# Kernel optimization log

Hardware: AMD Instinct MI355X
Metric: run time of the kernel (lower is better)

## Reference

```python
import jax, jax.numpy as jnp
import numpy as np

INPUT_SIZE = 1024
OUTPUT_SIZE = 1024
B, S = 4, 2048


def setup_inputs() -> dict:
    key = jax.random.key(0)
    k1, k2, k3, k4, k5, k6 = jax.random.split(key, 6)
    scale = 1.0 / np.sqrt(INPUT_SIZE)
    return {
        "inputs_for_keys": jax.random.normal(k1, (B, S, INPUT_SIZE), jnp.float32),
        "inputs_for_values": jax.random.normal(k2, (B, S, INPUT_SIZE), jnp.float32),
        "inputs_for_queries": jax.random.normal(k3, (B, S, INPUT_SIZE), jnp.float32),
        "W_k": jax.random.normal(k4, (INPUT_SIZE, OUTPUT_SIZE), jnp.float32) * scale,
        "W_v": jax.random.normal(k5, (INPUT_SIZE, OUTPUT_SIZE), jnp.float32) * scale,
        "W_q": jax.random.normal(k6, (INPUT_SIZE, OUTPUT_SIZE), jnp.float32) * scale,
    }


def reference(inputs_for_keys, inputs_for_values, inputs_for_queries, W_k, W_v, W_q):
    # Linear projections (bias=False): x @ W  -> [B, S, D_out]
    K = jnp.einsum("bsi,io->bso", inputs_for_keys, W_k)
    V = jnp.einsum("bsi,io->bso", inputs_for_values, W_v)
    Q = jnp.einsum("bqi,io->bqo", inputs_for_queries, W_q)
    d_k = K.shape[-1]
    # scores: [B, Sq, Sk], scaled by sqrt(embedding_size of K)
    scores = jnp.einsum("bqd,bkd->bqk", Q, K) / jnp.sqrt(jnp.asarray(d_k, Q.dtype))
    # causal mask: positions k > q masked to -inf (use_mask=True since is_self_attention)
    q_idx = jnp.arange(Q.shape[1])[:, None]
    k_idx = jnp.arange(K.shape[1])[None, :]
    scores = jnp.where(k_idx > q_idx, jnp.asarray(-jnp.inf, scores.dtype), scores)
    weights = jax.nn.softmax(scores, axis=-1)
    # output: [B, Sq, D_out]
    return jnp.einsum("bqk,bkd->bqd", weights, V)
```

## Files before the change

### kernel.cpp

```cpp
#include <hip/hip_runtime.h>


typedef __attribute__((ext_vector_type(8))) short short8;
typedef __attribute__((ext_vector_type(4))) float floatx4;

static constexpr long long XE = 8388608LL;
static constexpr long long WE = 1048576LL;

static __device__ __forceinline__ unsigned short f2b(float f) {
  unsigned u = __builtin_bit_cast(unsigned, f);
  u = (u + 0x7fffu + ((u >> 16) & 1u)) >> 16;
  return (unsigned short)u;
}

static __device__ __forceinline__ void gload16(const unsigned short* g, unsigned short* l) {
  __builtin_amdgcn_global_load_lds(
      (const __attribute__((address_space(1))) unsigned int*)g,
      (__attribute__((address_space(3))) unsigned int*)l, 16, 0, 0);
}

#define VMCNT(n) asm volatile("s_waitcnt vmcnt(" #n ")" ::: "memory")
#define LGKM0() asm volatile("s_waitcnt lgkmcnt(0)" ::: "memory")
#define BARRIER() do { asm volatile("" ::: "memory"); __builtin_amdgcn_s_barrier(); asm volatile("" ::: "memory"); } while (0)

#define STAGE(base, matoff, h, slot, kt) do {                                  \
    const unsigned short* _s = (base) + (h) * 131072 + (kt) * 64;              \
    char* _d = sb + (slot) * 65536 + (matoff) + (h) * 16384 + dwave;           \
    gload16(_s, (unsigned short*)_d);                                          \
    gload16(_s + 65536, (unsigned short*)(_d + 8192));                         \
  } while (0)

#define READ_A(slot, mb) do {                                                  \
    const char* _p = sb + (slot) * 65536 + aoffb + (mb) * 2048;                \
    af[0][0] = *(const short8*)(_p + c0);        af[0][1] = *(const short8*)(_p + c1); \
    af[1][0] = *(const short8*)(_p + 2048 + c0); af[1][1] = *(const short8*)(_p + 2048 + c1); \
    af[2][0] = *(const short8*)(_p + 4096 + c0); af[2][1] = *(const short8*)(_p + 4096 + c1); \
    af[3][0] = *(const short8*)(_p + 6144 + c0); af[3][1] = *(const short8*)(_p + 6144 + c1); \
  } while (0)

#define READ_B(slot, nb, bfx) do {                                             \
    const char* _p = sb + (slot) * 65536 + boffb + (nb) * 2048;                \
    bfx[0][0] = *(const short8*)(_p + c0);        bfx[0][1] = *(const short8*)(_p + c1); \
    bfx[1][0] = *(const short8*)(_p + 2048 + c0); bfx[1][1] = *(const short8*)(_p + 2048 + c1); \
  } while (0)

#define MF16(MB, NB, bfx) do {                                                 \
    __builtin_amdgcn_s_setprio(1);                                             \
    _Pragma("unroll")                                                          \
    for (int _m = 0; _m < 4; ++_m) {                                           \
      _Pragma("unroll")                                                        \
      for (int _n = 0; _n < 2; ++_n) {                                         \
        acc[(MB) + _m][(NB) + _n] = __builtin_amdgcn_mfma_f32_16x16x32_bf16(   \
            af[_m][0], bfx[_n][0], acc[(MB) + _m][(NB) + _n], 0, 0, 0);        \
        acc[(MB) + _m][(NB) + _n] = __builtin_amdgcn_mfma_f32_16x16x32_bf16(   \
            af[_m][1], bfx[_n][1], acc[(MB) + _m][(NB) + _n], 0, 0, 0);        \
      } }                                                                      \
    __builtin_amdgcn_s_setprio(0);                                             \
  } while (0)

__global__ __launch_bounds__(512, 2) void projTV8(
    const unsigned short* __restrict__ Xb, const unsigned short* __restrict__ WvT,
    const unsigned short* __restrict__ Gt, unsigned short* __restrict__ Tb,
    unsigned short* __restrict__ Vt) {
  extern __shared__ char sb[];
  const int orig = blockIdx.x;
  const int w = (orig & 7) * 32 + (orig >> 3);
  const unsigned short *Aop, *Bop;
  unsigned short* C;
  int ldc, bi, bj;
  if (w < 128) { Aop = Xb + XE; Bop = Gt; C = Tb; ldc = 1024; bi = w >> 2; bj = w & 3; }
  else { const int j = w - 128; Aop = WvT; Bop = Xb; C = Vt; ldc = 8192; bi = j & 3; bj = j >> 2; }

  const int tid = threadIdx.x, wave = tid >> 6, lane = tid & 63;
  const int wm = wave >> 2, wn = wave & 3, frow = lane & 15, hi = lane >> 4;
  const int r0 = tid >> 3, p0 = ((tid & 7) ^ (r0 & 7)) * 8;
  const int dwave = wave * 1024;
  const int sx = frow & 7;
  const int c0 = (hi ^ sx) * 16, c1 = ((4 + hi) ^ sx) * 16;
  const int aoffb = (wm * 128 + frow) * 128;
  const int boffb = 32768 + (wn * 64 + frow) * 128;
  const unsigned short* Ab = Aop + (long long)(bi * 256 + r0) * 1024 + p0;
  const unsigned short* Bb = Bop + (long long)(bj * 256 + r0) * 1024 + p0;

  short8 af[4][2], bf0[2][2], bf1[2][2];
  floatx4 acc[8][4] = {};

  STAGE(Ab, 0, 0, 0, 0);     STAGE(Ab, 0, 1, 0, 0);
  STAGE(Bb, 32768, 0, 0, 0); STAGE(Bb, 32768, 1, 0, 0);
  STAGE(Bb, 32768, 0, 1, 1); STAGE(Bb, 32768, 1, 1, 1);
  VMCNT(4);
  BARRIER();

  for (int t = 0; t < 8; ++t) {
    const int kt1 = 2 * t + 1, kt2 = 2 * t + 2, kt3 = 2 * t + 3;
    const bool pf = t < 7;
    READ_A(0, 0); READ_B(0, 0, bf0);
    STAGE(Ab, 0, 0, 1, kt1);
    BARRIER(); LGKM0();
    MF16(0, 0, bf0);
    BARRIER();
    READ_B(0, 2, bf1);
    STAGE(Ab, 0, 1, 1, kt1);
    BARRIER(); LGKM0();
    MF16(0, 2, bf1);
    BARRIER();
    READ_A(0, 4);
    if (pf) STAGE(Bb, 32768, 0, 0, kt2);
    BARRIER(); LGKM0();
    MF16(4, 2, bf1);
    BARRIER();
    if (pf) STAGE(Bb, 32768, 1, 0, kt2);
    BARRIER();
    MF16(4, 0, bf0);
    if (pf) { VMCNT(4); } else { VMCNT(0); }
    BARRIER();
    READ_A(1, 0); READ_B(1, 0, bf0);
    if (pf) STAGE(Ab, 0, 0, 0, kt2);
    BARRIER(); LGKM0();
    MF16(0, 0, bf0);
    BARRIER();
    READ_B(1, 2, bf1);
    if (pf) STAGE(Ab, 0, 1, 0, kt2);
    BARRIER(); LGKM0();
    MF16(0, 2, bf1);
    BARRIER();
    READ_A(1, 4);
    if (pf) STAGE(Bb, 32768, 0, 1, kt3);
    BARRIER(); LGKM0();
    MF16(4, 2, bf1);
    BARRIER();
    if (pf) STAGE(Bb, 32768, 1, 1, kt3);
    BARRIER();
    MF16(4, 0, bf0);
    if (pf) { VMCNT(4); } else { VMCNT(0); }
    BARRIER();
  }

  const long long crow0 = (long long)bi * 256 + wm * 128 + hi * 4;
  const int ccol = bj * 256 + wn * 64 + frow;
#pragma unroll
  for (int m = 0; m < 8; ++m)
#pragma unroll
    for (int j = 0; j < 4; ++j) {
      unsigned short* cp = C + (crow0 + m * 16 + j) * (long long)ldc + ccol;
#pragma unroll
      for (int n = 0; n < 4; ++n) cp[n * 16] = f2b(acc[m][n][j]);
    }
}

template <int NF>
static __device__ __forceinline__ void gemm_loop(
    const unsigned short* __restrict__ A, const unsigned short* __restrict__ Bt,
    int lda, int ldb, int nk, int bi, int bj,
    unsigned short* lA, unsigned short* lB, floatx4 acc[4][NF]) {
  const int t = threadIdx.x, wave = t >> 6, lane = t & 63;
  const int wr = wave >> 1, wc = wave & 1;
  const int sr = lane >> 3;
  const int sc = ((lane & 7) ^ sr) * 8;
  const unsigned short* gA = A + (long long)(bi * 128 + wave * 32 + sr) * lda + sc;
  const unsigned short* gB = Bt + (long long)(bj * (NF * 32) + wave * (NF * 8) + sr) * ldb + sc;
  unsigned short* lAw = lA + wave * 2048;
  unsigned short* lBw = lB + wave * (NF * 512);
  const int frow = lane & 15, hi = lane >> 4;

  for (int ks = 0; ks < nk; ++ks) {
    const long long k0 = (long long)ks * 64;
    __syncthreads();
#pragma unroll
    for (int g = 0; g < 4; ++g)
      gload16(gA + (long long)g * 8 * lda + k0, lAw + g * 512);
#pragma unroll
    for (int g = 0; g < NF; ++g)
      gload16(gB + (long long)g * 8 * ldb + k0, lBw + g * 512);
    __syncthreads();
#pragma unroll
    for (int kk = 0; kk < 2; ++kk) {
      const int ch = (kk * 4 + hi) ^ (frow & 7);
      short8 af[4], bf[NF];
#pragma unroll
      for (int m = 0; m < 4; ++m)
        af[m] = *(const short8*)&lA[(wr * 64 + m * 16 + frow) * 64 + ch * 8];
#pragma unroll
      for (int n = 0; n < NF; ++n)
        bf[n] = *(const short8*)&lB[(wc * (NF * 16) + n * 16 + frow) * 64 + ch * 8];
#pragma unroll
      for (int m = 0; m < 4; ++m)
#pragma unroll
        for (int n = 0; n < NF; ++n)
          acc[m][n] = __builtin_amdgcn_mfma_f32_16x16x32_bf16(af[m], bf[n], acc[m][n], 0, 0, 0);
    }
  }
}

__global__ __launch_bounds__(256) void gt_kernel(
    const unsigned short* __restrict__ WkB, const unsigned short* __restrict__ WqB,
    unsigned short* __restrict__ Gt) {
  __shared__ __align__(16) unsigned short lA[8192], lB[8192];
  floatx4 acc[4][4] = {};
  gemm_loop<4>(WkB, WqB, 1024, 1024, 16, blockIdx.x, blockIdx.y, lA, lB, acc);
  const int tid = threadIdx.x, wave = tid >> 6, lane = tid & 63;
  const int wr = wave >> 1, wc = wave & 1, frow = lane & 15, hi = lane >> 4;
  const long long crow0 = (long long)blockIdx.x * 128 + wr * 64 + hi * 4;
  const int ccol = blockIdx.y * 128 + wc * 64 + frow;
#pragma unroll
  for (int m = 0; m < 4; ++m)
#pragma unroll
    for (int j = 0; j < 4; ++j) {
      unsigned short* cp = Gt + (crow0 + m * 16 + j) * 1024 + ccol;
#pragma unroll
      for (int n = 0; n < 4; ++n) cp[n * 16] = f2b(acc[m][n][j]);
    }
}

__global__ __launch_bounds__(256) void scores_exp(
    const unsigned short* __restrict__ Tb, const unsigned short* __restrict__ Xk,
    unsigned short* __restrict__ P, float* __restrict__ Rpart) {
  __shared__ __align__(16) unsigned short lA[8192], lB[4096];
  const int orig = blockIdx.x;
  const int w = (orig & 7) * 136 + (orig >> 3);
  const int b = w / 272;
  int t2 = w - b * 272;
  int bi = 0;
  while (t2 >= 2 * bi + 2) { t2 -= 2 * bi + 2; ++bi; }
  const int bj = t2;

  floatx4 acc[4][2] = {};
  gemm_loop<2>(Tb + (long long)b * 2048 * 1024, Xk + (long long)b * 2048 * 1024,
               1024, 1024, 16, bi, bj, lA, lB, acc);

  const int tid = threadIdx.x, wave = tid >> 6, lane = tid & 63;
  const int wr = wave >> 1, wc = wave & 1, frow = lane & 15, hi = lane >> 4;
  const bool diag = (bj >= 2 * bi);
  float rp[4][4];
#pragma unroll
  for (int m = 0; m < 4; ++m)
#pragma unroll
    for (int j = 0; j < 4; ++j) {
      const int rloc = wr * 64 + hi * 4 + m * 16 + j;
      const int rglob = bi * 128 + rloc;
      float s = 0.f;
#pragma unroll
      for (int n = 0; n < 2; ++n) {
        const int cglob = bj * 64 + wc * 32 + n * 16 + frow;
        float e = __expf(acc[m][n][j] * 0.03125f);
        if (diag && cglob > rglob) e = 0.f;
        acc[m][n][j] = e;
        s += e;
      }
      rp[m][j] = s;
    }
#pragma unroll
  for (int m = 0; m < 4; ++m)
#pragma unroll
    for (int j = 0; j < 4; ++j) {
      rp[m][j] += __shfl_xor(rp[m][j], 1);
      rp[m][j] += __shfl_xor(rp[m][j], 2);
      rp[m][j] += __shfl_xor(rp[m][j], 4);
      rp[m][j] += __shfl_xor(rp[m][j], 8);
    }
  unsigned short* C = P + (long long)b * 2048 * 2048;
  const long long crow0 = (long long)bi * 128 + wr * 64 + hi * 4;
  const int ccol = bj * 64 + wc * 32 + frow;
#pragma unroll
  for (int m = 0; m < 4; ++m)
#pragma unroll
    for (int j = 0; j < 4; ++j) {
      unsigned short* cp = C + (crow0 + m * 16 + j) * 2048LL + ccol;
      cp[0] = f2b(acc[m][0][j]);
      cp[16] = f2b(acc[m][1][j]);
    }
  __syncthreads();
  float* red = (float*)lA;
  if (frow == 0) {
#pragma unroll
    for (int m = 0; m < 4; ++m)
#pragma unroll
      for (int j = 0; j < 4; ++j)
        red[(wr * 64 + hi * 4 + m * 16 + j) * 2 + wc] = rp[m][j];
  }
  __syncthreads();
  if (tid < 128)
    Rpart[((long long)b * 32 + bj) * 2048 + bi * 128 + tid] = red[tid * 2] + red[tid * 2 + 1];
}

__global__ __launch_bounds__(256) void rowsum(
    const float* __restrict__ Rpart, float* __restrict__ Rinv) {
  const int t = blockIdx.x * 256 + threadIdx.x;
  const int b = t >> 11, row = t & 2047;
  const int nb = (row >> 6) + 1;
  float s = 0.f;
  for (int bj = 0; bj < nb; ++bj) s += Rpart[(b * 32 + bj) * 2048 + row];
  Rinv[t] = 1.f / s;
}

__global__ __launch_bounds__(256) void pv_kernel(
    const unsigned short* __restrict__ P, const unsigned short* __restrict__ Vt,
    const float* __restrict__ Rinv, float* __restrict__ out) {
  __shared__ __align__(16) unsigned short lA[8192], lB[4096];
  const int orig = blockIdx.x;
  const int c = orig & 7, i = orig >> 3;
  const int bi = 15 - (i >> 3);
  const int rr = (i & 7) + c * 8;
  const int b = rr >> 4, bj = rr & 15;
  floatx4 acc[4][2] = {};
  gemm_loop<2>(P + (long long)b * 2048 * 2048, Vt + (long long)b * 2048, 2048, 8192,
               (bi + 1) * 2, bi, bj, lA, lB, acc);
  const int tid = threadIdx.x, wave = tid >> 6, lane = tid & 63;
  const int wr = wave >> 1, wc = wave & 1, frow = lane & 15, hi = lane >> 4;
  float* C = out + (long long)b * 2048 * 1024;
  const float* Ri = Rinv + b * 2048;
#pragma unroll
  for (int m = 0; m < 4; ++m)
#pragma unroll
    for (int j = 0; j < 4; ++j) {
      const int row = bi * 128 + wr * 64 + hi * 4 + m * 16 + j;
      const float riv = Ri[row];
      float* cp = C + (long long)row * 1024 + bj * 64 + wc * 32 + frow;
      cp[0] = acc[m][0][j] * riv;
      cp[16] = acc[m][1][j] * riv;
    }
}

__global__ __launch_bounds__(256) void cvtAll(
    const float* __restrict__ Xk, const float* __restrict__ Xv,
    const float* __restrict__ Xq, const float* __restrict__ Wq,
    const float* __restrict__ Wk, const float* __restrict__ Wv,
    unsigned short* __restrict__ Xb, unsigned short* __restrict__ WqB,
    unsigned short* __restrict__ WkB, unsigned short* __restrict__ WvT) {
  __shared__ unsigned short tile[64][65];
  const int bx = blockIdx.x, t = threadIdx.x;
  if (bx < 1536) {
    const int y = bx / 512, sub = bx - y * 512;
    const float* in = y == 0 ? Xv : (y == 1 ? Xq : Xk);
    unsigned short* o = Xb + (long long)y * XE;
    const int n8 = (int)(XE / 8), stride = 512 * 256;
    for (int i = sub * 256 + t; i < n8; i += stride) {
      float4 a = ((const float4*)in)[2 * i];
      float4 d = ((const float4*)in)[2 * i + 1];
      short8 v;
      v[0] = (short)f2b(a.x); v[1] = (short)f2b(a.y);
      v[2] = (short)f2b(a.z); v[3] = (short)f2b(a.w);
      v[4] = (short)f2b(d.x); v[5] = (short)f2b(d.y);
      v[6] = (short)f2b(d.z); v[7] = (short)f2b(d.w);
      ((short8*)o)[i] = v;
    }
  } else if (bx < 1792) {
    const int w2 = bx - 1536;
    const int y = w2 >> 7, sub = w2 & 127;
    const float* in = y == 0 ? Wq : Wk;
    unsigned short* o = y == 0 ? WqB : WkB;
    const int n8 = (int)(WE / 8), stride = 128 * 256;
    for (int i = sub * 256 + t; i < n8; i += stride) {
      float4 a = ((const float4*)in)[2 * i];
      float4 d = ((const float4*)in)[2 * i + 1];
      short8 v;
      v[0] = (short)f2b(a.x); v[1] = (short)f2b(a.y);
      v[2] = (short)f2b(a.z); v[3] = (short)f2b(a.w);
      v[4] = (short)f2b(d.x); v[5] = (short)f2b(d.y);
      v[6] = (short)f2b(d.z); v[7] = (short)f2b(d.w);
      ((short8*)o)[i] = v;
    }
  } else {
    const int v = bx - 1792;
    const int i0 = (v & 15) * 64, j0 = (v >> 4) * 64;
#pragma unroll
    for (int r = 0; r < 16; ++r) {
      int lin = r * 256 + t;
      int i = lin >> 6, j = lin & 63;
      tile[i][j] = f2b(Wv[(long long)(i0 + i) * 1024 + j0 + j]);
    }
    __syncthreads();
#pragma unroll
    for (int r = 0; r < 16; ++r) {
      int lin = r * 256 + t;
      int o = lin >> 6, i = lin & 63;
      WvT[(long long)(j0 + o) * 1024 + i0 + i] = tile[i][o];
    }
  }
}

extern "C" void kernel_launch(void* const* d_in, const int* in_sizes, int n_in,
                              void* d_out, int out_size, void* d_ws, size_t ws_size,
                              hipStream_t stream) {
  const float* Xk = (const float*)d_in[0];
  const float* Xv = (const float*)d_in[1];
  const float* Xq = (const float*)d_in[2];
  const float* Wk = (const float*)d_in[3];
  const float* Wv = (const float*)d_in[4];
  const float* Wq = (const float*)d_in[5];
  float* out = (float*)d_out;

  unsigned short* ws = (unsigned short*)d_ws;
  unsigned short* Xb = ws;
  unsigned short* WqB = ws + 3 * XE;
  unsigned short* WkB = WqB + WE;
  unsigned short* WvT = WkB + WE;
  unsigned short* Gt = WvT + WE;
  unsigned short* Tb = Gt + WE;
  unsigned short* Vt = Tb + XE;
  float* Rpart = (float*)(Vt + XE);
  float* Rinv = Rpart + 4 * 32 * 2048;
  unsigned short* Pbuf = ws;

  cvtAll<<<2048, 256, 0, stream>>>(Xk, Xv, Xq, Wq, Wk, Wv, Xb, WqB, WkB, WvT);
  gt_kernel<<<dim3(8, 8), 256, 0, stream>>>(WkB, WqB, Gt);
  projTV8<<<256, 512, 131072, stream>>>(Xb, WvT, Gt, Tb, Vt);
  scores_exp<<<1088, 256, 0, stream>>>(Tb, Xb + 2 * XE, Pbuf, Rpart);
  rowsum<<<32, 256, 0, stream>>>(Rpart, Rinv);
  pv_kernel<<<1024, 256, 0, stream>>>(Pbuf, Vt, Rinv, out);
}
```

Before: 157.9 us.

## Widen PV output tile to 128 columns and process 16 elements per thread in conversion

The PV GEMM now computes a 128x128 output tile per block instead of 128x64 (gemm_loop<4>, a larger LDS B buffer, 512 blocks). Each P tile is therefore loaded half as often, cutting the redundant reads of the large probability matrix. The fp32-to-bf16 conversion kernel now handles 16 elements per thread iteration and uses fewer weight-conversion blocks. In exchange, PV has fewer blocks and more accumulator registers, which may lower occupancy and leave the triangular workload less evenly balanced.

```diff
diff --git a/kernel.cpp b/kernel.cpp
--- a/kernel.cpp
+++ b/kernel.cpp
@@ -296,14 +296,14 @@
 __global__ __launch_bounds__(256) void pv_kernel(
     const unsigned short* __restrict__ P, const unsigned short* __restrict__ Vt,
     const float* __restrict__ Rinv, float* __restrict__ out) {
-  __shared__ __align__(16) unsigned short lA[8192], lB[4096];
+  __shared__ __align__(16) unsigned short lA[8192], lB[8192];
   const int orig = blockIdx.x;
   const int c = orig & 7, i = orig >> 3;
-  const int bi = 15 - (i >> 3);
-  const int rr = (i & 7) + c * 8;
-  const int b = rr >> 4, bj = rr & 15;
-  floatx4 acc[4][2] = {};
-  gemm_loop<2>(P + (long long)b * 2048 * 2048, Vt + (long long)b * 2048, 2048, 8192,
+  const int bi = 15 - (i >> 2);
+  const int rr = (i & 3) + c * 4;
+  const int b = rr >> 3, bj = rr & 7;
+  floatx4 acc[4][4] = {};
+  gemm_loop<4>(P + (long long)b * 2048 * 2048, Vt + (long long)b * 2048, 2048, 8192,
                (bi + 1) * 2, bi, bj, lA, lB, acc);
   const int tid = threadIdx.x, wave = tid >> 6, lane = tid & 63;
   const int wr = wave >> 1, wc = wave & 1, frow = lane & 15, hi = lane >> 4;
@@ -315,9 +315,9 @@
     for (int j = 0; j < 4; ++j) {
       const int row = bi * 128 + wr * 64 + hi * 4 + m * 16 + j;
       const float riv = Ri[row];
-      float* cp = C + (long long)row * 1024 + bj * 64 + wc * 32 + frow;
-      cp[0] = acc[m][0][j] * riv;
-      cp[16] = acc[m][1][j] * riv;
+      float* cp = C + (long long)row * 1024 + bj * 128 + wc * 64 + frow;
+#pragma unroll
+      for (int n = 0; n < 4; ++n) cp[n * 16] = acc[m][n][j] * riv;
     }
 }
 
@@ -329,39 +329,39 @@
     unsigned short* __restrict__ WkB, unsigned short* __restrict__ WvT) {
   __shared__ unsigned short tile[64][65];
   const int bx = blockIdx.x, t = threadIdx.x;
-  if (bx < 1536) {
-    const int y = bx / 512, sub = bx - y * 512;
-    const float* in = y == 0 ? Xv : (y == 1 ? Xq : Xk);
-    unsigned short* o = Xb + (long long)y * XE;
-    const int n8 = (int)(XE / 8), stride = 512 * 256;
-    for (int i = sub * 256 + t; i < n8; i += stride) {
-      float4 a = ((const float4*)in)[2 * i];
-      float4 d = ((const float4*)in)[2 * i + 1];
-      short8 v;
-      v[0] = (short)f2b(a.x); v[1] = (short)f2b(a.y);
-      v[2] = (short)f2b(a.z); v[3] = (short)f2b(a.w);
-      v[4] = (short)f2b(d.x); v[5] = (short)f2b(d.y);
-      v[6] = (short)f2b(d.z); v[7] = (short)f2b(d.w);
-      ((short8*)o)[i] = v;
-    }
-  } else if (bx < 1792) {
-    const int w2 = bx - 1536;
-    const int y = w2 >> 7, sub = w2 & 127;
-    const float* in = y == 0 ? Wq : Wk;
-    unsigned short* o = y == 0 ? WqB : WkB;
-    const int n8 = (int)(WE / 8), stride = 128 * 256;
-    for (int i = sub * 256 + t; i < n8; i += stride) {
-      float4 a = ((const float4*)in)[2 * i];
-      float4 d = ((const float4*)in)[2 * i + 1];
-      short8 v;
-      v[0] = (short)f2b(a.x); v[1] = (short)f2b(a.y);
-      v[2] = (short)f2b(a.z); v[3] = (short)f2b(a.w);
-      v[4] = (short)f2b(d.x); v[5] = (short)f2b(d.y);
-      v[6] = (short)f2b(d.z); v[7] = (short)f2b(d.w);
-      ((short8*)o)[i] = v;
+  if (bx < 1664) {
+    const float* in;
+    unsigned short* o;
+    int n16, stride, idx0;
+    if (bx < 1536) {
+      const int y = bx / 512, sub = bx - y * 512;
+      in = y == 0 ? Xv : (y == 1 ? Xq : Xk);
+      o = Xb + (long long)y * XE;
+      n16 = (int)(XE / 16); stride = 512 * 256; idx0 = sub * 256 + t;
+    } else {
+      const int w2 = bx - 1536;
+      const int y = w2 >> 6, sub = w2 & 63;
+      in = y == 0 ? Wq : Wk;
+      o = y == 0 ? WqB : WkB;
+      n16 = (int)(WE / 16); stride = 64 * 256; idx0 = sub * 256 + t;
+    }
+    for (int i = idx0; i < n16; i += stride) {
+      const float4* src = (const float4*)in + 4 * (long long)i;
+      float4 a = src[0], b2 = src[1], c2 = src[2], d2 = src[3];
+      short8 v0, v1;
+      v0[0] = (short)f2b(a.x);  v0[1] = (short)f2b(a.y);
+      v0[2] = (short)f2b(a.z);  v0[3] = (short)f2b(a.w);
+      v0[4] = (short)f2b(b2.x); v0[5] = (short)f2b(b2.y);
+      v0[6] = (short)f2b(b2.z); v0[7] = (short)f2b(b2.w);
+      v1[0] = (short)f2b(c2.x); v1[1] = (short)f2b(c2.y);
+      v1[2] = (short)f2b(c2.z); v1[3] = (short)f2b(c2.w);
+      v1[4] = (short)f2b(d2.x); v1[5] = (short)f2b(d2.y);
+      v1[6] = (short)f2b(d2.z); v1[7] = (short)f2b(d2.w);
+      ((short8*)o)[2 * (long long)i] = v0;
+      ((short8*)o)[2 * (long long)i + 1] = v1;
     }
   } else {
-    const int v = bx - 1792;
+    const int v = bx - 1664;
     const int i0 = (v & 15) * 64, j0 = (v >> 4) * 64;
 #pragma unroll
     for (int r = 0; r < 16; ++r) {
@@ -402,10 +402,10 @@
   float* Rinv = Rpart + 4 * 32 * 2048;
   unsigned short* Pbuf = ws;
 
-  cvtAll<<<2048, 256, 0, stream>>>(Xk, Xv, Xq, Wq, Wk, Wv, Xb, WqB, WkB, WvT);
+  cvtAll<<<1920, 256, 0, stream>>>(Xk, Xv, Xq, Wq, Wk, Wv, Xb, WqB, WkB, WvT);
   gt_kernel<<<dim3(8, 8), 256, 0, stream>>>(WkB, WqB, Gt);
   projTV8<<<256, 512, 131072, stream>>>(Xb, WvT, Gt, Tb, Vt);
   scores_exp<<<1088, 256, 0, stream>>>(Tb, Xb + 2 * XE, Pbuf, Rpart);
   rowsum<<<32, 256, 0, stream>>>(Rpart, Rinv);
-  pv_kernel<<<1024, 256, 0, stream>>>(Pbuf, Vt, Rinv, out);
-}
+  pv_kernel<<<512, 256, 0, stream>>>(Pbuf, Vt, Rinv, out);
+}
```

Result: slower. 164.9 us (+4.4%).

## Use 256x256 eight-wave pipelined tile for causal scores-exp kernel

Applied to the files above, without the earlier changes.

Replaces the 128x64-tile scores kernel with one built on the same 256x256, 512-thread, 128KB-LDS pipelined K-loop used for the projection, factored into a shared macro. Only lower-triangular tile pairs are launched (144 blocks), and the row-sum partials shrink from 32 to 8 column blocks per row, so rowsum and the Rpart layout are adjusted to match. The aim is higher data reuse per block and better MFMA utilisation. In exchange, the grid is only 144 blocks on a GPU with many more CUs, and coarser 256-wide diagonal tiles compute more masked-out work.

```diff
diff --git a/kernel.cpp b/kernel.cpp
--- a/kernel.cpp
+++ b/kernel.cpp
@@ -58,6 +58,57 @@
     __builtin_amdgcn_s_setprio(0);                                             \
   } while (0)
 
+#define KLOOP8()                                                               \
+  STAGE(Ab, 0, 0, 0, 0);     STAGE(Ab, 0, 1, 0, 0);                            \
+  STAGE(Bb, 32768, 0, 0, 0); STAGE(Bb, 32768, 1, 0, 0);                        \
+  STAGE(Bb, 32768, 0, 1, 1); STAGE(Bb, 32768, 1, 1, 1);                        \
+  VMCNT(4);                                                                    \
+  BARRIER();                                                                   \
+  for (int t = 0; t < 8; ++t) {                                                \
+    const int kt1 = 2 * t + 1, kt2 = 2 * t + 2, kt3 = 2 * t + 3;               \
+    const bool pf = t < 7;                                                     \
+    READ_A(0, 0); READ_B(0, 0, bf0);                                           \
+    STAGE(Ab, 0, 0, 1, kt1);                                                   \
+    BARRIER(); LGKM0();                                                        \
+    MF16(0, 0, bf0);                                                           \
+    BARRIER();                                                                 \
+    READ_B(0, 2, bf1);                                                         \
+    STAGE(Ab, 0, 1, 1, kt1);                                                   \
+    BARRIER(); LGKM0();                                                        \
+    MF16(0, 2, bf1);                                                           \
+    BARRIER();                                                                 \
+    READ_A(0, 4);                                                              \
+    if (pf) STAGE(Bb, 32768, 0, 0, kt2);                                       \
+    BARRIER(); LGKM0();                                                        \
+    MF16(4, 2, bf1);                                                           \
+    BARRIER();                                                                 \
+    if (pf) STAGE(Bb, 32768, 1, 0, kt2);                                       \
+    BARRIER();                                                                 \
+    MF16(4, 0, bf0);                                                           \
+    if (pf) { VMCNT(4); } else { VMCNT(0); }                                   \
+    BARRIER();                                                                 \
+    READ_A(1, 0); READ_B(1, 0, bf0);                                           \
+    if (pf) STAGE(Ab, 0, 0, 0, kt2);                                           \
+    BARRIER(); LGKM0();                                                        \
+    MF16(0, 0, bf0);                                                           \
+    BARRIER();                                                                 \
+    READ_B(1, 2, bf1);                                                         \
+    if (pf) STAGE(Ab, 0, 1, 0, kt2);                                           \
+    BARRIER(); LGKM0();                                                        \
+    MF16(0, 2, bf1);                                                           \
+    BARRIER();                                                                 \
+    READ_A(1, 4);                                                              \
+    if (pf) STAGE(Bb, 32768, 0, 1, kt3);                                       \
+    BARRIER(); LGKM0();                                                        \
+    MF16(4, 2, bf1);                                                           \
+    BARRIER();                                                                 \
+    if (pf) STAGE(Bb, 32768, 1, 1, kt3);                                       \
+    BARRIER();                                                                 \
+    MF16(4, 0, bf0);                                                           \
+    if (pf) { VMCNT(4); } else { VMCNT(0); }                                   \
+    BARRIER();                                                                 \
+  }
+
 __global__ __launch_bounds__(512, 2) void projTV8(
     const unsigned short* __restrict__ Xb, const unsigned short* __restrict__ WvT,
     const unsigned short* __restrict__ Gt, unsigned short* __restrict__ Tb,
@@ -85,56 +136,7 @@
   short8 af[4][2], bf0[2][2], bf1[2][2];
   floatx4 acc[8][4] = {};
 
-  STAGE(Ab, 0, 0, 0, 0);     STAGE(Ab, 0, 1, 0, 0);
-  STAGE(Bb, 32768, 0, 0, 0); STAGE(Bb, 32768, 1, 0, 0);
-  STAGE(Bb, 32768, 0, 1, 1); STAGE(Bb, 32768, 1, 1, 1);
-  VMCNT(4);
-  BARRIER();
-
-  for (int t = 0; t < 8; ++t) {
-    const int kt1 = 2 * t + 1, kt2 = 2 * t + 2, kt3 = 2 * t + 3;
-    const bool pf = t < 7;
-    READ_A(0, 0); READ_B(0, 0, bf0);
-    STAGE(Ab, 0, 0, 1, kt1);
-    BARRIER(); LGKM0();
-    MF16(0, 0, bf0);
-    BARRIER();
-    READ_B(0, 2, bf1);
-    STAGE(Ab, 0, 1, 1, kt1);
-    BARRIER(); LGKM0();
-    MF16(0, 2, bf1);
-    BARRIER();
-    READ_A(0, 4);
-    if (pf) STAGE(Bb, 32768, 0, 0, kt2);
-    BARRIER(); LGKM0();
-    MF16(4, 2, bf1);
-    BARRIER();
-    if (pf) STAGE(Bb, 32768, 1, 0, kt2);
-    BARRIER();
-    MF16(4, 0, bf0);
-    if (pf) { VMCNT(4); } else { VMCNT(0); }
-    BARRIER();
-    READ_A(1, 0); READ_B(1, 0, bf0);
-    if (pf) STAGE(Ab, 0, 0, 0, kt2);
-    BARRIER(); LGKM0();
-    MF16(0, 0, bf0);
-    BARRIER();
-    READ_B(1, 2, bf1);
-    if (pf) STAGE(Ab, 0, 1, 0, kt2);
-    BARRIER(); LGKM0();
-    MF16(0, 2, bf1);
-    BARRIER();
-    READ_A(1, 4);
-    if (pf) STAGE(Bb, 32768, 0, 1, kt3);
-    BARRIER(); LGKM0();
-    MF16(4, 2, bf1);
-    BARRIER();
-    if (pf) STAGE(Bb, 32768, 1, 1, kt3);
-    BARRIER();
-    MF16(4, 0, bf0);
-    if (pf) { VMCNT(4); } else { VMCNT(0); }
-    BARRIER();
-  }
+  KLOOP8();
 
   const long long crow0 = (long long)bi * 256 + wm * 128 + hi * 4;
   const int ccol = bj * 256 + wn * 64 + frow;
@@ -146,6 +148,77 @@
 #pragma unroll
       for (int n = 0; n < 4; ++n) cp[n * 16] = f2b(acc[m][n][j]);
     }
+}
+
+__global__ __launch_bounds__(512, 2) void scores_exp8(
+    const unsigned short* __restrict__ Tb, const unsigned short* __restrict__ Xk,
+    unsigned short* __restrict__ P, float* __restrict__ Rpart) {
+  extern __shared__ char sb[];
+  const int orig = blockIdx.x;
+  const int w = (orig & 7) * 18 + (orig >> 3);
+  const int b = w / 36;
+  int t2 = w - b * 36;
+  int bi = 0;
+  while (t2 >= bi + 1) { t2 -= bi + 1; ++bi; }
+  const int bj = t2;
+
+  const unsigned short* Aop = Tb + (long long)b * 2048 * 1024;
+  const unsigned short* Bop = Xk + (long long)b * 2048 * 1024;
+
+  const int tid = threadIdx.x, wave = tid >> 6, lane = tid & 63;
+  const int wm = wave >> 2, wn = wave & 3, frow = lane & 15, hi = lane >> 4;
+  const int r0 = tid >> 3, p0 = ((tid & 7) ^ (r0 & 7)) * 8;
+  const int dwave = wave * 1024;
+  const int sx = frow & 7;
+  const int c0 = (hi ^ sx) * 16, c1 = ((4 + hi) ^ sx) * 16;
+  const int aoffb = (wm * 128 + frow) * 128;
+  const int boffb = 32768 + (wn * 64 + frow) * 128;
+  const unsigned short* Ab = Aop + (long long)(bi * 256 + r0) * 1024 + p0;
+  const unsigned short* Bb = Bop + (long long)(bj * 256 + r0) * 1024 + p0;
+
+  short8 af[4][2], bf0[2][2], bf1[2][2];
+  floatx4 acc[8][4] = {};
+
+  KLOOP8();
+
+  const bool diag = (bi == bj);
+  unsigned short* C = P + (long long)b * 2048 * 2048;
+  float rs[8][4];
+#pragma unroll
+  for (int m = 0; m < 8; ++m)
+#pragma unroll
+    for (int j = 0; j < 4; ++j) {
+      const int row_loc = wm * 128 + hi * 4 + m * 16 + j;
+      const int row_glob = bi * 256 + row_loc;
+      unsigned short* cp = C + (long long)row_glob * 2048 + bj * 256 + wn * 64 + frow;
+      float s = 0.f;
+#pragma unroll
+      for (int n = 0; n < 4; ++n) {
+        const int col = bj * 256 + wn * 64 + n * 16 + frow;
+        float e = __expf(acc[m][n][j] * 0.03125f);
+        if (diag && col > row_glob) e = 0.f;
+        cp[n * 16] = f2b(e);
+        s += e;
+      }
+      s += __shfl_xor(s, 1);
+      s += __shfl_xor(s, 2);
+      s += __shfl_xor(s, 4);
+      s += __shfl_xor(s, 8);
+      rs[m][j] = s;
+    }
+  __syncthreads();
+  float* red = (float*)sb;
+  if (frow == 0) {
+#pragma unroll
+    for (int m = 0; m < 8; ++m)
+#pragma unroll
+      for (int j = 0; j < 4; ++j)
+        red[(wm * 128 + hi * 4 + m * 16 + j) * 4 + wn] = rs[m][j];
+  }
+  __syncthreads();
+  if (tid < 256)
+    Rpart[((long long)b * 8 + bj) * 2048 + bi * 256 + tid] =
+        red[tid * 4] + red[tid * 4 + 1] + red[tid * 4 + 2] + red[tid * 4 + 3];
 }
 
 template <int NF>
@@ -212,84 +285,13 @@
     }
 }
 
-__global__ __launch_bounds__(256) void scores_exp(
-    const unsigned short* __restrict__ Tb, const unsigned short* __restrict__ Xk,
-    unsigned short* __restrict__ P, float* __restrict__ Rpart) {
-  __shared__ __align__(16) unsigned short lA[8192], lB[4096];
-  const int orig = blockIdx.x;
-  const int w = (orig & 7) * 136 + (orig >> 3);
-  const int b = w / 272;
-  int t2 = w - b * 272;
-  int bi = 0;
-  while (t2 >= 2 * bi + 2) { t2 -= 2 * bi + 2; ++bi; }
-  const int bj = t2;
-
-  floatx4 acc[4][2] = {};
-  gemm_loop<2>(Tb + (long long)b * 2048 * 1024, Xk + (long long)b * 2048 * 1024,
-               1024, 1024, 16, bi, bj, lA, lB, acc);
-
-  const int tid = threadIdx.x, wave = tid >> 6, lane = tid & 63;
-  const int wr = wave >> 1, wc = wave & 1, frow = lane & 15, hi = lane >> 4;
-  const bool diag = (bj >= 2 * bi);
-  float rp[4][4];
-#pragma unroll
-  for (int m = 0; m < 4; ++m)
-#pragma unroll
-    for (int j = 0; j < 4; ++j) {
-      const int rloc = wr * 64 + hi * 4 + m * 16 + j;
-      const int rglob = bi * 128 + rloc;
-      float s = 0.f;
-#pragma unroll
-      for (int n = 0; n < 2; ++n) {
-        const int cglob = bj * 64 + wc * 32 + n * 16 + frow;
-        float e = __expf(acc[m][n][j] * 0.03125f);
-        if (diag && cglob > rglob) e = 0.f;
-        acc[m][n][j] = e;
-        s += e;
-      }
-      rp[m][j] = s;
-    }
-#pragma unroll
-  for (int m = 0; m < 4; ++m)
-#pragma unroll
-    for (int j = 0; j < 4; ++j) {
-      rp[m][j] += __shfl_xor(rp[m][j], 1);
-      rp[m][j] += __shfl_xor(rp[m][j], 2);
-      rp[m][j] += __shfl_xor(rp[m][j], 4);
-      rp[m][j] += __shfl_xor(rp[m][j], 8);
-    }
-  unsigned short* C = P + (long long)b * 2048 * 2048;
-  const long long crow0 = (long long)bi * 128 + wr * 64 + hi * 4;
-  const int ccol = bj * 64 + wc * 32 + frow;
-#pragma unroll
-  for (int m = 0; m < 4; ++m)
-#pragma unroll
-    for (int j = 0; j < 4; ++j) {
-      unsigned short* cp = C + (crow0 + m * 16 + j) * 2048LL + ccol;
-      cp[0] = f2b(acc[m][0][j]);
-      cp[16] = f2b(acc[m][1][j]);
-    }
-  __syncthreads();
-  float* red = (float*)lA;
-  if (frow == 0) {
-#pragma unroll
-    for (int m = 0; m < 4; ++m)
-#pragma unroll
-      for (int j = 0; j < 4; ++j)
-        red[(wr * 64 + hi * 4 + m * 16 + j) * 2 + wc] = rp[m][j];
-  }
-  __syncthreads();
-  if (tid < 128)
-    Rpart[((long long)b * 32 + bj) * 2048 + bi * 128 + tid] = red[tid * 2] + red[tid * 2 + 1];
-}
-
 __global__ __launch_bounds__(256) void rowsum(
     const float* __restrict__ Rpart, float* __restrict__ Rinv) {
   const int t = blockIdx.x * 256 + threadIdx.x;
   const int b = t >> 11, row = t & 2047;
-  const int nb = (row >> 6) + 1;
+  const int nb = (row >> 8) + 1;
   float s = 0.f;
-  for (int bj = 0; bj < nb; ++bj) s += Rpart[(b * 32 + bj) * 2048 + row];
+  for (int bj = 0; bj < nb; ++bj) s += Rpart[(b * 8 + bj) * 2048 + row];
   Rinv[t] = 1.f / s;
 }
 
@@ -399,13 +401,13 @@
   unsigned short* Tb = Gt + WE;
   unsigned short* Vt = Tb + XE;
   float* Rpart = (float*)(Vt + XE);
-  float* Rinv = Rpart + 4 * 32 * 2048;
+  float* Rinv = Rpart + 4 * 8 * 2048;
   unsigned short* Pbuf = ws;
 
   cvtAll<<<2048, 256, 0, stream>>>(Xk, Xv, Xq, Wq, Wk, Wv, Xb, WqB, WkB, WvT);
   gt_kernel<<<dim3(8, 8), 256, 0, stream>>>(WkB, WqB, Gt);
   projTV8<<<256, 512, 131072, stream>>>(Xb, WvT, Gt, Tb, Vt);
-  scores_exp<<<1088, 256, 0, stream>>>(Tb, Xb + 2 * XE, Pbuf, Rpart);
+  scores_exp8<<<144, 512, 131072, stream>>>(Tb, Xb + 2 * XE, Pbuf, Rpart);
   rowsum<<<32, 256, 0, stream>>>(Rpart, Rinv);
   pv_kernel<<<1024, 256, 0, stream>>>(Pbuf, Vt, Rinv, out);
 }
```

After: 150.1 us, median of 2. -4.9%, faster.
